# Kernel tuning notes

Hardware: AMD Instinct MI355X
Metric: run time of the kernel (lower is better)

Reference implementation:

```python
import jax, jax.numpy as jnp
import numpy as np

EPS = 1e-5

def setup_inputs() -> dict:
    key = jax.random.key(0)
    ks = jax.random.split(key, 8)
    b, c, p, h = 8, 128, 2048, 4
    inp = {
        "input": jax.random.normal(ks[0], (b, c, p), jnp.float32),
        "gamma": jnp.ones((c,), jnp.float32),
        "beta": jnp.zeros((c,), jnp.float32),
        "Wq": jax.random.normal(ks[1], (c * h, c), jnp.float32) * (c ** -0.5),
        "bq": jnp.zeros((c * h,), jnp.float32),
        "Wk": jax.random.normal(ks[2], (c * h, c), jnp.float32) * (c ** -0.5),
        "bk": jnp.zeros((c * h,), jnp.float32),
        "Wv": jax.random.normal(ks[3], (c * h, c), jnp.float32) * (c ** -0.5),
        "bv": jnp.zeros((c * h,), jnp.float32),
        "Wo": jax.random.normal(ks[4], (c, c * h), jnp.float32) * ((c * h) ** -0.5),
        "bo": jnp.zeros((c,), jnp.float32),
    }
    return inp


def reference(input, gamma, beta, Wq, bq, Wk, bk, Wv, bv, Wo, bo):
    b, c, p = input.shape
    h = Wq.shape[0] // c
    # BatchNorm1d (training-mode batch stats): mean/var per channel over (batch, points)
    mean = jnp.mean(input, axis=(0, 2), keepdims=True)          # [1,c,1]
    var = jnp.mean((input - mean) ** 2, axis=(0, 2), keepdims=True)
    x = (input - mean) * jax.lax.rsqrt(var + EPS)
    x = x * gamma[None, :, None] + beta[None, :, None]
    # 1x1 conv projections == channel matmuls; then split c*h -> (c, h)
    q = (jnp.einsum('oc,bcp->bop', Wq, x) + bq[None, :, None]).reshape(b, c, h, p)
    k = (jnp.einsum('oc,bcp->bop', Wk, x) + bk[None, :, None]).reshape(b, c, h, p)
    v = (jnp.einsum('oc,bcp->bop', Wv, x) + bv[None, :, None]).reshape(b, c, h, p)
    # attention over points; scale by c**-0.5
    weight = jnp.einsum('bchi,bchj->bhij', q, k) * (c ** -0.5)   # [b,h,p,p]
    weight = jax.nn.softmax(weight, axis=3)
    att = jnp.einsum('bhij,bchj->bchi', weight, v)               # [b,c,h,p]
    att = att.reshape(b, c * h, p)
    out = jnp.einsum('oc,bcp->bop', Wo, att) + bo[None, :, None]
    return out + input
```

## Files before the change

### kernel.cpp

```cpp
#include <hip/hip_runtime.h>
#include <hip/hip_bf16.h>

#define NB 8
#define NC 128
#define NP 2048
#define NH 4
#define NCH 512

typedef __attribute__((ext_vector_type(8))) short bf16x8;
typedef __attribute__((ext_vector_type(16))) float f32x16;

__device__ __forceinline__ float bf2f(unsigned short u) {
  return __uint_as_float(((unsigned)u) << 16);
}
__device__ __forceinline__ unsigned short f2bf(float f) {
  __hip_bfloat16 h = __float2bfloat16(f);
  return *reinterpret_cast<unsigned short*>(&h);
}
__device__ __forceinline__ unsigned pk2(float lo, float hi) {
  return (unsigned)f2bf(lo) | ((unsigned)f2bf(hi) << 16);
}
__device__ __forceinline__ void gload_lds16(const void* g, void* l) {
  __builtin_amdgcn_global_load_lds(
      (const __attribute__((address_space(1))) void*)g,
      (__attribute__((address_space(3))) void*)l, 16, 0, 0);
}
__device__ __forceinline__ void plswap(unsigned& a, unsigned& b) {
  asm volatile("v_permlane32_swap_b32 %0, %1" : "+v"(a), "+v"(b));
}

__global__ __launch_bounds__(256) void bn_partial(
    const float* __restrict__ in, float* __restrict__ psum,
    float* __restrict__ psum2) {
  int c = blockIdx.x >> 2, qtr = blockIdx.x & 3;
  int t = threadIdx.x;
  float s = 0.f, s2 = 0.f;
  for (int b = 0; b < NB; ++b) {
    const float* ptr = in + ((size_t)b * NC + c) * NP + qtr * 512;
    #pragma unroll
    for (int p = 0; p < 2; ++p) {
      float v = ptr[p * 256 + t];
      s += v; s2 += v * v;
    }
  }
  for (int off = 32; off; off >>= 1) {
    s += __shfl_down(s, off, 64);
    s2 += __shfl_down(s2, off, 64);
  }
  __shared__ float red[8];
  int lane = t & 63, wid = t >> 6;
  if (!lane) { red[wid] = s; red[wid + 4] = s2; }
  __syncthreads();
  if (!t) {
    psum[blockIdx.x] = red[0] + red[1] + red[2] + red[3];
    psum2[blockIdx.x] = red[4] + red[5] + red[6] + red[7];
  }
}

__global__ __launch_bounds__(512, 2) void qkv_proj(
    const float* __restrict__ in, const float* __restrict__ gamma,
    const float* __restrict__ beta, const float* __restrict__ psum,
    const float* __restrict__ psum2, const float* __restrict__ Wq,
    const float* __restrict__ bq, const float* __restrict__ Wk,
    const float* __restrict__ bk, const float* __restrict__ Wv,
    const float* __restrict__ bv, unsigned short* __restrict__ qws,
    unsigned short* __restrict__ kws, unsigned short* __restrict__ vws) {
  __shared__ float sc[128], sh[128], bias[1536];
  __shared__ __align__(16) unsigned short Xt[64][136];
  int t = threadIdx.x;
  int pt = blockIdx.x & 31, b = blockIdx.x >> 5;
  int p0 = pt * 64;
  if (t < 128) {
    float s = psum[t * 4] + psum[t * 4 + 1] + psum[t * 4 + 2] + psum[t * 4 + 3];
    float s2 = psum2[t * 4] + psum2[t * 4 + 1] + psum2[t * 4 + 2] + psum2[t * 4 + 3];
    const float invn = 1.f / (NB * NP);
    float mean = s * invn, var = s2 * invn - mean * mean;
    float scl = gamma[t] * rsqrtf(var + 1e-5f);
    sc[t] = scl; sh[t] = beta[t] - mean * scl;
  }
  bias[t] = bq[t]; bias[512 + t] = bk[t]; bias[1024 + t] = bv[t];
  __syncthreads();
  {
    int p = t & 63, c0 = (t >> 6) * 16;
    const float* src = in + ((size_t)b * NC + c0) * NP + p0 + p;
    #pragma unroll
    for (int cc = 0; cc < 16; ++cc) {
      float v = src[(size_t)cc * NP];
      Xt[p][c0 + cc] = f2bf(v * sc[c0 + cc] + sh[c0 + cc]);
    }
  }
  __syncthreads();
  int w = t >> 6, lane = t & 63, l31 = lane & 31, h5 = lane >> 5;
  #pragma unroll 1
  for (int s = 0; s < 3; ++s) {
    int strip = s * 8 + w;
    int proj = strip >> 3, within = (strip & 7) * 64;
    const float* W = proj == 0 ? Wq : (proj == 1 ? Wk : Wv);
    f32x16 acc[2][2] = {};
    #pragma unroll
    for (int ks = 0; ks < 8; ++ks) {
      bf16x8 af[2], bf[2];
      #pragma unroll
      for (int mt = 0; mt < 2; ++mt) {
        const float* wr = W + (size_t)(within + mt * 32 + l31) * NC + ks * 16 + h5 * 8;
        float4 a = *(const float4*)wr, b4 = *(const float4*)(wr + 4);
        union { bf16x8 v; unsigned u[4]; } uu;
        uu.u[0] = pk2(a.x, a.y); uu.u[1] = pk2(a.z, a.w);
        uu.u[2] = pk2(b4.x, b4.y); uu.u[3] = pk2(b4.z, b4.w);
        af[mt] = uu.v;
      }
      #pragma unroll
      for (int nt = 0; nt < 2; ++nt)
        bf[nt] = *(const bf16x8*)&Xt[nt * 32 + l31][ks * 16 + h5 * 8];
      if (proj < 2) {
        #pragma unroll
        for (int mt = 0; mt < 2; ++mt)
          #pragma unroll
          for (int nt = 0; nt < 2; ++nt)
            acc[mt][nt] = __builtin_amdgcn_mfma_f32_32x32x16_bf16(bf[nt], af[mt], acc[mt][nt], 0, 0, 0);
      } else {
        #pragma unroll
        for (int mt = 0; mt < 2; ++mt)
          #pragma unroll
          for (int nt = 0; nt < 2; ++nt)
            acc[mt][nt] = __builtin_amdgcn_mfma_f32_32x32x16_bf16(af[mt], bf[nt], acc[mt][nt], 0, 0, 0);
      }
    }
    if (proj < 2) {
      unsigned short* dst = proj == 0 ? qws : kws;
      float qs = proj == 0 ? 0.12751743762765621f : 1.0f;
      #pragma unroll
      for (int mt = 0; mt < 2; ++mt) {
        int o = within + mt * 32 + l31;
        float bs = bias[proj * 512 + o];
        int c = o >> 2;
        int g = ((c & ~7) << 2) + ((o & 3) << 3) + (c & 7);
        unsigned short* drow = dst + (size_t)b * NP * NCH + g;
        #pragma unroll
        for (int nt = 0; nt < 2; ++nt)
          #pragma unroll
          for (int r = 0; r < 16; ++r) {
            int p = p0 + nt * 32 + (r & 3) + 8 * (r >> 2) + 4 * h5;
            drow[(size_t)p * NCH] = f2bf((acc[mt][nt][r] + bs) * qs);
          }
      }
    } else {
      #pragma unroll
      for (int mt = 0; mt < 2; ++mt)
        #pragma unroll
        for (int nt = 0; nt < 2; ++nt)
          #pragma unroll
          for (int r = 0; r < 16; ++r) {
            int oo = within + mt * 32 + (r & 3) + 8 * (r >> 2) + 4 * h5;
            float val = acc[mt][nt][r] + bias[1024 + oo];
            vws[((size_t)(b * NCH + oo)) * NP + p0 + nt * 32 + l31] = f2bf(val);
          }
    }
  }
}

__global__ __launch_bounds__(256, 2) void attn(
    const unsigned short* __restrict__ qT, const unsigned short* __restrict__ kT,
    const unsigned short* __restrict__ vws, unsigned short* __restrict__ attws) {
  __shared__ uint4 Kbuf[2][1024];
  __shared__ uint4 Vbuf[2][1024];
  int tid = threadIdx.x;
  int wl = tid >> 6, lane = tid & 63, l31 = lane & 31, h5 = lane >> 5;
  int bid = blockIdx.x;
  int head = bid & 31, it = bid >> 5;
  int b = head >> 2, hh = head & 3;
  int i0 = it * 128;
  const unsigned short* kb = kT + (size_t)b * NP * NCH;
  const unsigned short* vb = vws + (size_t)b * NCH * NP;

  int t4 = tid >> 4;
  int ch = (tid & 15) ^ (t4 & 15);
  size_t vO = ((size_t)((t4 * 2 + (ch >> 3)) * 4 + hh)) * NP + (ch & 7) * 8;

  auto stage = [&](int bi, int j0v) {
    #pragma unroll
    for (int k = 0; k < 4; ++k) {
      gload_lds16(kb + (size_t)(j0v + k * 16 + t4) * NCH + ch * 32 + hh * 8,
                  &Kbuf[bi][k * 256 + tid]);
      gload_lds16(vb + vO + (size_t)k * 128 * NP + j0v,
                  &Vbuf[bi][k * 256 + tid]);
    }
  };

  bf16x8 qf[8];
  {
    const unsigned short* qp =
        qT + ((size_t)b * NP + (i0 + wl * 32 + l31)) * NCH + h5 * 32 + hh * 8;
    #pragma unroll
    for (int ks = 0; ks < 8; ++ks) qf[ks] = *(const bf16x8*)(qp + ks * 64);
  }

  f32x16 oacc[4] = {};
  float lsum = 0.f;

  stage(0, 0);
  __syncthreads();

  int kbase = l31 * 16, ksw = l31 & 15;
  #pragma unroll 1
  for (int tI = 0; tI < 32; ++tI) {
    int cur = tI & 1;
    if (tI < 31) stage(cur ^ 1, (tI + 1) * 64);

    f32x16 sacT0 = {}, sacT1 = {};
    #pragma unroll
    for (int ks = 0; ks < 8; ++ks) {
      int cidx = (ks * 2 + h5) ^ ksw;
      bf16x8 kf0 = *(const bf16x8*)&Kbuf[cur][kbase + cidx];
      bf16x8 kf1 = *(const bf16x8*)&Kbuf[cur][512 + kbase + cidx];
      sacT0 = __builtin_amdgcn_mfma_f32_32x32x16_bf16(kf0, qf[ks], sacT0, 0, 0, 0);
      sacT1 = __builtin_amdgcn_mfma_f32_32x32x16_bf16(kf1, qf[ks], sacT1, 0, 0, 0);
    }
    bf16x8 pfrag[4];
    #pragma unroll
    for (int ntj = 0; ntj < 2; ++ntj) {
      f32x16& sacT = ntj ? sacT1 : sacT0;
      #pragma unroll
      for (int r = 0; r < 16; ++r) {
        sacT[r] = __builtin_amdgcn_exp2f(sacT[r]);
        lsum += sacT[r];
      }
      unsigned wv[8];
      #pragma unroll
      for (int q = 0; q < 8; ++q) wv[q] = pk2(sacT[q * 2], sacT[q * 2 + 1]);
      plswap(wv[0], wv[2]); plswap(wv[1], wv[3]);
      plswap(wv[4], wv[6]); plswap(wv[5], wv[7]);
      union { bf16x8 v; unsigned u[4]; } f0, f1;
      f0.u[0] = wv[0]; f0.u[1] = wv[1]; f0.u[2] = wv[2]; f0.u[3] = wv[3];
      f1.u[0] = wv[4]; f1.u[1] = wv[5]; f1.u[2] = wv[6]; f1.u[3] = wv[7];
      pfrag[ntj * 2] = f0.v; pfrag[ntj * 2 + 1] = f1.v;
    }
    #pragma unroll
    for (int ntc = 0; ntc < 4; ++ntc) {
      int r = ntc * 16 + (l31 >> 1);
      int rb = r * 16, r15 = r & 15, c8 = (l31 & 1) * 8;
      #pragma unroll
      for (int kw = 0; kw < 4; ++kw) {
        bf16x8 vf = *(const bf16x8*)&Vbuf[cur][rb + ((c8 + kw * 2 + h5) ^ r15)];
        oacc[ntc] = __builtin_amdgcn_mfma_f32_32x32x16_bf16(vf, pfrag[kw], oacc[ntc], 0, 0, 0);
      }
    }
    __syncthreads();
  }

  float linv = 1.0f / (lsum + __shfl_xor(lsum, 32, 64));
  unsigned short* TB = (unsigned short*)Kbuf;
  int iL = wl * 32 + l31;
  int isw = iL & 7;
  #pragma unroll
  for (int ntc = 0; ntc < 4; ++ntc)
    #pragma unroll
    for (int r = 0; r < 16; ++r) {
      int c = ntc * 32 + (r & 3) + 8 * (r >> 2) + 4 * h5;
      TB[iL * 128 + (((c >> 3) ^ isw) << 3) + (c & 7)] = f2bf(oacc[ntc][r] * linv);
    }
  __syncthreads();
  {
    int i2 = tid >> 1, half = tid & 1;
    unsigned short* gp = attws + ((size_t)b * NP + i0 + i2) * NCH + hh * 128 + half * 64;
    const unsigned short* rp = TB + i2 * 128;
    int sw2 = i2 & 7;
    #pragma unroll
    for (int q = 0; q < 8; ++q) {
      int ck = half * 8 + q;
      uint4 v = *(const uint4*)(rp + ((ck ^ sw2) << 3));
      *(uint4*)(gp + q * 8) = v;
    }
  }
}

__global__ __launch_bounds__(256) void wo_perm(
    const float* __restrict__ Wo, unsigned short* __restrict__ WoP) {
  int idx = (blockIdx.x * 256 + threadIdx.x) * 4;
  int o = idx >> 9, g0 = idx & 511;
  int hh = g0 >> 7;
  const float* src = Wo + (size_t)o * NCH + (g0 & 127) * 4 + hh;
  union { unsigned short u[4]; uint2 v; } tmp;
  #pragma unroll
  for (int e = 0; e < 4; ++e) tmp.u[e] = f2bf(src[e * 4]);
  *(uint2*)(WoP + idx) = tmp.v;
}

__global__ __launch_bounds__(256, 2) void out_proj(
    const unsigned short* __restrict__ attT, const unsigned short* __restrict__ WoP,
    const float* __restrict__ bo, const float* __restrict__ in,
    float* __restrict__ out) {
  __shared__ uint4 Abuf[2][512];
  int t = threadIdx.x;
  int pt = blockIdx.x & 63, b = blockIdx.x >> 6;
  int p0 = pt * 32;
  int w = t >> 6, lane = t & 63, l31 = lane & 31, h5 = lane >> 5;
  const unsigned short* ab = attT + (size_t)b * NP * NCH;
  int row0 = t >> 4, pos = t & 15;
  auto stage = [&](int bi, int k0) {
    #pragma unroll
    for (int q = 0; q < 2; ++q) {
      int row = q * 16 + row0;
      int chq = pos ^ (row & 15);
      gload_lds16(ab + ((size_t)(p0 + row)) * NCH + k0 * 128 + chq * 8,
                  &Abuf[bi][q * 256 + t]);
    }
  };
  f32x16 acc = {};
  stage(0, 0);
  __syncthreads();
  #pragma unroll 1
  for (int k0 = 0; k0 < 4; ++k0) {
    int cur = k0 & 1;
    if (k0 < 3) stage(cur ^ 1, k0 + 1);
    #pragma unroll
    for (int ks = 0; ks < 8; ++ks) {
      bf16x8 af = *(const bf16x8*)(WoP + (size_t)(w * 32 + l31) * NCH + k0 * 128 + ks * 16 + h5 * 8);
      bf16x8 bf = *(const bf16x8*)&Abuf[cur][l31 * 16 + ((ks * 2 + h5) ^ (l31 & 15))];
      acc = __builtin_amdgcn_mfma_f32_32x32x16_bf16(af, bf, acc, 0, 0, 0);
    }
    __syncthreads();
  }
  #pragma unroll
  for (int r = 0; r < 16; ++r) {
    int o = w * 32 + (r & 3) + 8 * (r >> 2) + 4 * h5;
    int p = p0 + l31;
    size_t idx = ((size_t)(b * NC + o)) * NP + p;
    out[idx] = acc[r] + bo[o] + in[idx];
  }
}

extern "C" void kernel_launch(void* const* d_in, const int* in_sizes, int n_in,
                              void* d_out, int out_size, void* d_ws, size_t ws_size,
                              hipStream_t stream) {
  const float* in    = (const float*)d_in[0];
  const float* gamma = (const float*)d_in[1];
  const float* beta  = (const float*)d_in[2];
  const float* Wq = (const float*)d_in[3];
  const float* bq = (const float*)d_in[4];
  const float* Wk = (const float*)d_in[5];
  const float* bk = (const float*)d_in[6];
  const float* Wv = (const float*)d_in[7];
  const float* bv = (const float*)d_in[8];
  const float* Wo = (const float*)d_in[9];
  const float* bo = (const float*)d_in[10];
  float* out = (float*)d_out;

  char* ws = (char*)d_ws;
  float* psum  = (float*)ws;
  float* psum2 = psum + 512;
  const size_t QKV_ELEMS = (size_t)NB * NCH * NP;
  unsigned short* qws   = (unsigned short*)(ws + 8192);
  unsigned short* kws   = qws + QKV_ELEMS;
  unsigned short* vws   = kws + QKV_ELEMS;
  unsigned short* attws = vws + QKV_ELEMS;
  unsigned short* WoP   = qws;

  bn_partial<<<dim3(512), dim3(256), 0, stream>>>(in, psum, psum2);
  qkv_proj<<<dim3(256), dim3(512), 0, stream>>>(
      in, gamma, beta, psum, psum2, Wq, bq, Wk, bk, Wv, bv, qws, kws, vws);
  attn<<<dim3(512), dim3(256), 0, stream>>>(qws, kws, vws, attws);
  wo_perm<<<dim3(64), dim3(256), 0, stream>>>(Wo, WoP);
  out_proj<<<dim3(512), dim3(256), 0, stream>>>(attws, WoP, bo, in, out);
}
```

Before: 210.4 us.

## Store Q/K head-major via LDS transpose for coalesced writes and reads

Q and K projections are now staged through a swizzled shared-memory tile and written as contiguous 16-byte vectors in a per-(batch,head) [P][C] layout, replacing scattered 2-byte stores with a large row stride. The attention kernel's Q fragment loads and K staging addresses are updated to read this head-major layout, so each head's data is contiguous. The change adds a 32 KB shared buffer and extra barriers to the projection kernel, which may lower its occupancy.

```diff
diff --git a/kernel.cpp b/kernel.cpp
--- a/kernel.cpp
+++ b/kernel.cpp
@@ -67,6 +67,7 @@
     unsigned short* __restrict__ kws, unsigned short* __restrict__ vws) {
   __shared__ float sc[128], sh[128], bias[1536];
   __shared__ __align__(16) unsigned short Xt[64][136];
+  __shared__ __align__(16) unsigned short Tq[32][512];
   int t = threadIdx.x;
   int pt = blockIdx.x & 31, b = blockIdx.x >> 5;
   int p0 = pt * 64;
@@ -130,19 +131,31 @@
       unsigned short* dst = proj == 0 ? qws : kws;
       float qs = proj == 0 ? 0.12751743762765621f : 1.0f;
       #pragma unroll
-      for (int mt = 0; mt < 2; ++mt) {
-        int o = within + mt * 32 + l31;
-        float bs = bias[proj * 512 + o];
-        int c = o >> 2;
-        int g = ((c & ~7) << 2) + ((o & 3) << 3) + (c & 7);
-        unsigned short* drow = dst + (size_t)b * NP * NCH + g;
-        #pragma unroll
-        for (int nt = 0; nt < 2; ++nt)
+      for (int nt = 0; nt < 2; ++nt) {
+        __syncthreads();
+        #pragma unroll
+        for (int mt = 0; mt < 2; ++mt) {
+          int o = within + mt * 32 + l31;
+          float bs = bias[proj * 512 + o];
+          int c = o >> 2, hh = o & 3;
+          int colb = hh * 128 + ((((c >> 3) ^ hh) << 3) | (c & 7));
           #pragma unroll
           for (int r = 0; r < 16; ++r) {
-            int p = p0 + nt * 32 + (r & 3) + 8 * (r >> 2) + 4 * h5;
-            drow[(size_t)p * NCH] = f2bf((acc[mt][nt][r] + bs) * qs);
+            int pl = (r & 3) + 8 * (r >> 2) + 4 * h5;
+            Tq[pl][colb] = f2bf((acc[mt][nt][r] + bs) * qs);
           }
+        }
+        __syncthreads();
+        int ri = t >> 2, qt = t & 3;
+        int pl = ri >> 2, hh = ri & 3;
+        unsigned short* gp = dst +
+            ((size_t)(b * 4 + hh) * NP + (p0 + nt * 32 + pl)) * NC + qt * 32;
+        const unsigned short* rp = &Tq[pl][hh * 128];
+        #pragma unroll
+        for (int q = 0; q < 4; ++q) {
+          int ck = qt * 4 + q;
+          *(uint4*)(gp + q * 8) = *(const uint4*)(rp + ((ck ^ hh) << 3));
+        }
       }
     } else {
       #pragma unroll
@@ -170,7 +183,7 @@
   int head = bid & 31, it = bid >> 5;
   int b = head >> 2, hh = head & 3;
   int i0 = it * 128;
-  const unsigned short* kb = kT + (size_t)b * NP * NCH;
+  const unsigned short* krow = kT + (size_t)(b * 4 + hh) * NP * NC;
   const unsigned short* vb = vws + (size_t)b * NCH * NP;
 
   int t4 = tid >> 4;
@@ -180,7 +193,7 @@
   auto stage = [&](int bi, int j0v) {
     #pragma unroll
     for (int k = 0; k < 4; ++k) {
-      gload_lds16(kb + (size_t)(j0v + k * 16 + t4) * NCH + ch * 32 + hh * 8,
+      gload_lds16(krow + (size_t)(j0v + k * 16 + t4) * NC + (ch << 3),
                   &Kbuf[bi][k * 256 + tid]);
       gload_lds16(vb + vO + (size_t)k * 128 * NP + j0v,
                   &Vbuf[bi][k * 256 + tid]);
@@ -190,9 +203,9 @@
   bf16x8 qf[8];
   {
     const unsigned short* qp =
-        qT + ((size_t)b * NP + (i0 + wl * 32 + l31)) * NCH + h5 * 32 + hh * 8;
-    #pragma unroll
-    for (int ks = 0; ks < 8; ++ks) qf[ks] = *(const bf16x8*)(qp + ks * 64);
+        qT + ((size_t)(b * 4 + hh) * NP + (i0 + wl * 32 + l31)) * NC + h5 * 8;
+    #pragma unroll
+    for (int ks = 0; ks < 8; ++ks) qf[ks] = *(const bf16x8*)(qp + ks * 16);
   }
 
   f32x16 oacc[4] = {};
```

Result: faster. 206.2 us (-2.0%).
